# Optimization experiments

Hardware: AMD Instinct MI355X
Metric: run time of the kernel (lower is better)

Reference implementation:

```python
import jax, jax.numpy as jnp
import numpy as np
from jax import lax

ALPHA = 0.3          # opt['retrieval_strategy']['margin']
NB_SAMPLES = 10      # hardest negatives kept per anchor
W_IRR = 1.0
W_RII = 1.0
B = 4096
D = 1024
NB_CLASSES = 1048


def _pairwise_dist(x, y):
    # Euclidean pairwise distance matrix [B, B] (self.dist in the torch module)
    x2 = jnp.sum(x * x, axis=1, keepdims=True)          # [B,1]
    y2 = jnp.sum(y * y, axis=1, keepdims=True).T        # [1,B]
    d2 = x2 + y2 - 2.0 * (x @ y.T)
    return jnp.sqrt(jnp.maximum(d2, 0.0))


def setup_inputs() -> dict:
    key = jax.random.key(0)
    k1, k2, k3, k4 = jax.random.split(key, 4)
    input1 = jax.random.normal(k1, (B, D), dtype=jnp.float32)
    input2 = jax.random.normal(k2, (B, D), dtype=jnp.float32)
    # target==1 everywhere -> 'matches' mask selects the whole batch (identity gather)
    target = jnp.ones((B, 1), dtype=jnp.int32)
    # classes in [1, NB_CLASSES) -> all rows valid (class != 0)
    class1 = jax.random.randint(k3, (B, 1), 1, NB_CLASSES, dtype=jnp.int32)
    class2 = jax.random.randint(k4, (B, 1), 1, NB_CLASSES, dtype=jnp.int32)
    return {"input1": input1, "input2": input2, "target": target,
            "class1": class1, "class2": class2}


def _mine(cost):
    # calculate_cost with sampling='max_negative': sort rows descending, keep nb_samples.
    # top_k == descending sort truncated to k.
    top, _ = lax.top_k(cost, NB_SAMPLES)                # [B, NB_SAMPLES]
    return top


def reference(input1, input2, target, class1, class2):
    # matches = (target == 1) is all-true by construction -> instance_* = full inputs
    dist = _pairwise_dist(input1, input2)               # [B, B]
    diag = jnp.diagonal(dist)                           # [B]
    n = dist.shape[0]
    eye = jnp.eye(n, dtype=bool)

    # IRR: anchor image, positive its own recipe, negatives other recipes
    cost_irr = jnp.maximum(diag[:, None] - dist + ALPHA, 0.0)
    cost_irr = jnp.where(eye, 0.0, cost_irr)
    top_irr = _mine(cost_irr)
    bad_irr = jnp.mean((top_irr == 0.0).astype(jnp.float32))
    loss_irr = top_irr.mean() * W_IRR

    # RII: anchor recipe, positive its own image, negatives other images (cost.t())
    cost_rii = jnp.maximum(diag[None, :] - dist + ALPHA, 0.0)
    cost_rii = jnp.where(eye, 0.0, cost_rii)
    top_rii = _mine(cost_rii.T)
    bad_rii = jnp.mean((top_rii == 0.0).astype(jnp.float32))
    loss_rii = top_rii.mean() * W_RII

    return jnp.stack([loss_irr, loss_rii, bad_irr, bad_rii])
```

## Files before the change

### kernel.cpp

```cpp
#include <hip/hip_runtime.h>
#include <hip/hip_fp16.h>

#define ALPHA 0.3f
#define B_SZ 4096
#define D_SZ 1024
#define CT_STRIDE 137
#define BIGF 3.0e38f

typedef __attribute__((ext_vector_type(8))) _Float16 half8;
typedef __attribute__((ext_vector_type(4))) _Float16 half4;
typedef __attribute__((ext_vector_type(4))) float floatx4;

typedef __attribute__((address_space(1))) const void* gas_t;
typedef __attribute__((address_space(3))) void* las_t;

__device__ __forceinline__ float wave_reduce_add(float v) {
#pragma unroll
    for (int off = 32; off; off >>= 1) v += __shfl_xor(v, off);
    return v;
}

__device__ __forceinline__ void insert10(float (&best)[10], float x) {
#pragma unroll
    for (int p = 0; p < 10; ++p) {
        float lo = fminf(best[p], x);
        x = fmaxf(best[p], x);
        best[p] = lo;
    }
}

__global__ void __launch_bounds__(256) prep_kernel(
    const float* __restrict__ in1, const float* __restrict__ in2,
    _Float16* __restrict__ Xh, _Float16* __restrict__ Yh,
    float* __restrict__ x2, float* __restrict__ y2, float* __restrict__ mth) {
    int row = blockIdx.x;
    int t = threadIdx.x;
    const float4* a4 = (const float4*)(in1 + (size_t)row * D_SZ);
    const float4* b4 = (const float4*)(in2 + (size_t)row * D_SZ);
    float4 a = a4[t], b = b4[t];
    half4 ha = {(_Float16)a.x, (_Float16)a.y, (_Float16)a.z, (_Float16)a.w};
    half4 hb = {(_Float16)b.x, (_Float16)b.y, (_Float16)b.z, (_Float16)b.w};
    ((half4*)(Xh + (size_t)row * D_SZ))[t] = ha;
    ((half4*)(Yh + (size_t)row * D_SZ))[t] = hb;
    float sa = a.x * a.x + a.y * a.y + a.z * a.z + a.w * a.w;
    float sb = b.x * b.x + b.y * b.y + b.z * b.z + b.w * b.w;
    float d0 = a.x - b.x, d1 = a.y - b.y, d2v = a.z - b.z, d3 = a.w - b.w;
    float sd = d0 * d0 + d1 * d1 + d2v * d2v + d3 * d3;
    sa = wave_reduce_add(sa);
    sb = wave_reduce_add(sb);
    sd = wave_reduce_add(sd);
    __shared__ float red[3][4];
    int wave = t >> 6, lane = t & 63;
    if (lane == 0) { red[0][wave] = sa; red[1][wave] = sb; red[2][wave] = sd; }
    __syncthreads();
    if (t == 0) {
        x2[row] = red[0][0] + red[0][1] + red[0][2] + red[0][3];
        y2[row] = red[1][0] + red[1][1] + red[1][2] + red[1][3];
        mth[row] = sqrtf(red[2][0] + red[2][1] + red[2][2] + red[2][3]) + ALPHA;
    }
}

__global__ void __launch_bounds__(256, 4) gemm_topk_kernel(
    const _Float16* __restrict__ Xh, const _Float16* __restrict__ Yh,
    const float* __restrict__ x2, const float* __restrict__ y2,
    float* __restrict__ CandI, float* __restrict__ CandR) {
    __shared__ _Float16 smem[128 * CT_STRIDE];
    _Float16* As = smem;
    _Float16* Bs = smem + 4096;
    int tid = threadIdx.x;
    int wave = tid >> 6, lane = tid & 63;
    int waveR = wave >> 1, waveC = wave & 1;
    int bx = blockIdx.x, by = blockIdx.y;
    int q = lane >> 4, mrow = lane & 15;

    floatx4 acc[4][4] = {};

    int c0 = tid, c1 = 256 + tid;
    int r0 = c0 >> 2, q0 = (c0 & 3) ^ ((r0 >> 1) & 3);
    int r1 = c1 >> 2, q1 = (c1 & 3) ^ ((r1 >> 1) & 3);
    const _Float16* gA0 = Xh + (size_t)(by * 128 + r0) * D_SZ + q0 * 8;
    const _Float16* gB0 = Yh + (size_t)(bx * 128 + r0) * D_SZ + q0 * 8;
    const _Float16* gA1 = Xh + (size_t)(by * 128 + r1) * D_SZ + q1 * 8;
    const _Float16* gB1 = Yh + (size_t)(bx * 128 + r1) * D_SZ + q1 * 8;
    _Float16* la0 = &As[(wave * 64) * 8];
    _Float16* lb0 = &Bs[(wave * 64) * 8];
    _Float16* la1 = &As[(256 + wave * 64) * 8];
    _Float16* lb1 = &Bs[(256 + wave * 64) * 8];

    int aoff[4], boff[4];
#pragma unroll
    for (int mi = 0; mi < 4; ++mi) {
        int R = waveR * 64 + mi * 16 + mrow;
        aoff[mi] = R * 32 + (q ^ ((R >> 1) & 3)) * 8;
    }
#pragma unroll
    for (int ni = 0; ni < 4; ++ni) {
        int R = waveC * 64 + ni * 16 + mrow;
        boff[ni] = R * 32 + (q ^ ((R >> 1) & 3)) * 8;
    }

    for (int k0 = 0; k0 < D_SZ; k0 += 32) {
        __syncthreads();
        __builtin_amdgcn_global_load_lds((gas_t)(const void*)(gA0 + k0), (las_t)(void*)la0, 16, 0, 0);
        __builtin_amdgcn_global_load_lds((gas_t)(const void*)(gB0 + k0), (las_t)(void*)lb0, 16, 0, 0);
        __builtin_amdgcn_global_load_lds((gas_t)(const void*)(gA1 + k0), (las_t)(void*)la1, 16, 0, 0);
        __builtin_amdgcn_global_load_lds((gas_t)(const void*)(gB1 + k0), (las_t)(void*)lb1, 16, 0, 0);
        __syncthreads();
        half8 af[4], bf[4];
#pragma unroll
        for (int mi = 0; mi < 4; ++mi) af[mi] = *(const half8*)&As[aoff[mi]];
#pragma unroll
        for (int ni = 0; ni < 4; ++ni) bf[ni] = *(const half8*)&Bs[boff[ni]];
#pragma unroll
        for (int mi = 0; mi < 4; ++mi)
#pragma unroll
            for (int ni = 0; ni < 4; ++ni)
                acc[mi][ni] = __builtin_amdgcn_mfma_f32_16x16x32_f16(af[mi], bf[ni], acc[mi][ni], 0, 0, 0);
    }
    __syncthreads();

    _Float16* Ct = smem;
#pragma unroll
    for (int ni = 0; ni < 4; ++ni) {
        int lc = waveC * 64 + ni * 16 + mrow;
        float y2v = y2[bx * 128 + lc];
#pragma unroll
        for (int mi = 0; mi < 4; ++mi) {
            int lr0 = waveR * 64 + mi * 16 + q * 4;
            int gr0 = by * 128 + lr0;
            floatx4 v = acc[mi][ni];
            Ct[(lr0 + 0) * CT_STRIDE + lc] = (_Float16)(x2[gr0 + 0] + y2v - 2.0f * v[0]);
            Ct[(lr0 + 1) * CT_STRIDE + lc] = (_Float16)(x2[gr0 + 1] + y2v - 2.0f * v[1]);
            Ct[(lr0 + 2) * CT_STRIDE + lc] = (_Float16)(x2[gr0 + 2] + y2v - 2.0f * v[2]);
            Ct[(lr0 + 3) * CT_STRIDE + lc] = (_Float16)(x2[gr0 + 3] + y2v - 2.0f * v[3]);
        }
    }
    __syncthreads();

    {
        int rloc = wave * 32 + (lane & 31);
        int chalf = lane >> 5;
        int grow = by * 128 + rloc;
        int diagc = grow - bx * 128;
        float best[10];
#pragma unroll
        for (int i = 0; i < 10; ++i) best[i] = BIGF;
#pragma unroll 8
        for (int i = 0; i < 64; ++i) {
            int lc = chalf * 64 + i;
            float x = (float)Ct[rloc * CT_STRIDE + lc];
            if (lc == diagc) x = BIGF;
            insert10(best, x);
        }
        float* dst = CandI + ((size_t)grow * 32 + bx) * 20 + chalf * 10;
#pragma unroll
        for (int k = 0; k < 10; ++k) dst[k] = best[k];
    }

    {
        int cloc = wave * 32 + (lane & 31);
        int rhalf = lane >> 5;
        int gcol = bx * 128 + cloc;
        int diagr = gcol - by * 128;
        float best[10];
#pragma unroll
        for (int i = 0; i < 10; ++i) best[i] = BIGF;
#pragma unroll 8
        for (int i = 0; i < 64; ++i) {
            int lr = rhalf * 64 + i;
            float x = (float)Ct[lr * CT_STRIDE + cloc];
            if (lr == diagr) x = BIGF;
            insert10(best, x);
        }
        float* dst = CandR + ((size_t)gcol * 32 + by) * 20 + rhalf * 10;
#pragma unroll
        for (int k = 0; k < 10; ++k) dst[k] = best[k];
    }
}

__global__ void __launch_bounds__(256) merge_kernel(
    const float* __restrict__ CandI, const float* __restrict__ CandR,
    const float* __restrict__ mth,
    float* __restrict__ Srow, float* __restrict__ Zrow) {
    int wave = threadIdx.x >> 6, lane = threadIdx.x & 63;
    int r = blockIdx.x * 4 + wave;
    int row = r & (B_SZ - 1);
    const float* cp = ((r < B_SZ) ? CandI : CandR) + (size_t)row * 640;
    float best[10];
#pragma unroll
    for (int i = 0; i < 10; ++i) best[i] = BIGF;
#pragma unroll
    for (int j = 0; j < 10; ++j) insert10(best, cp[j * 64 + lane]);

    float mrow = mth[row];
    float s = 0.f, z = 0.f;
#pragma unroll
    for (int round = 0; round < 10; ++round) {
        float v0 = best[0];
        float g = v0;
#pragma unroll
        for (int off = 32; off; off >>= 1) g = fminf(g, __shfl_xor(g, off));
        unsigned long long ball = __ballot(v0 == g);
        int leader = __ffsll(ball) - 1;
        if (lane == leader) {
#pragma unroll
            for (int p = 0; p < 9; ++p) best[p] = best[p + 1];
            best[9] = BIGF;
        }
        float d = sqrtf(fmaxf(g, 0.f));
        float c = fmaxf(mrow - d, 0.f);
        s += c;
        z += (c == 0.f) ? 1.f : 0.f;
    }
    if (lane == 0) { Srow[r] = s; Zrow[r] = z; }
}

__global__ void __launch_bounds__(256) finalize_kernel(
    const float* __restrict__ Srow, const float* __restrict__ Zrow,
    float* __restrict__ out) {
    __shared__ float red[256][4];
    int t = threadIdx.x;
    float s0 = 0, s1 = 0, z0 = 0, z1 = 0;
#pragma unroll
    for (int k = 0; k < 8; ++k) {
        int i = k * 256 + t;
        float4 sv = ((const float4*)Srow)[i];
        float4 zv = ((const float4*)Zrow)[i];
        float ss = sv.x + sv.y + sv.z + sv.w;
        float zz = zv.x + zv.y + zv.z + zv.w;
        if (i < 1024) { s0 += ss; z0 += zz; } else { s1 += ss; z1 += zz; }
    }
    red[t][0] = s0; red[t][1] = s1; red[t][2] = z0; red[t][3] = z1;
    __syncthreads();
    for (int off = 128; off > 0; off >>= 1) {
        if (t < off) {
#pragma unroll
            for (int j = 0; j < 4; ++j) red[t][j] += red[t + off][j];
        }
        __syncthreads();
    }
    if (t == 0) {
        const float inv = 1.0f / (float)(B_SZ * 10);
        out[0] = red[0][0] * inv;
        out[1] = red[0][1] * inv;
        out[2] = red[0][2] * inv;
        out[3] = red[0][3] * inv;
    }
}

extern "C" void kernel_launch(void* const* d_in, const int* in_sizes, int n_in,
                              void* d_out, int out_size, void* d_ws, size_t ws_size,
                              hipStream_t stream) {
    const float* in1 = (const float*)d_in[0];
    const float* in2 = (const float*)d_in[1];
    float* out = (float*)d_out;

    char* ws = (char*)d_ws;
    const size_t MB = 1024 * 1024;
    _Float16* Xh = (_Float16*)(ws);
    _Float16* Yh = (_Float16*)(ws + 8 * MB);
    float* CandI = (float*)(ws + 16 * MB);
    float* CandR = (float*)(ws + 27 * MB);
    float* x2   = (float*)(ws + 38 * MB);
    float* y2   = x2 + B_SZ;
    float* mth  = y2 + B_SZ;
    float* Srow = mth + B_SZ;
    float* Zrow = Srow + 2 * B_SZ;
    const size_t needed = 38 * MB + (size_t)(3 * B_SZ + 4 * B_SZ) * sizeof(float);
    if (ws_size < needed) return;

    hipLaunchKernelGGL(prep_kernel, dim3(B_SZ), dim3(256), 0, stream,
                       in1, in2, Xh, Yh, x2, y2, mth);
    hipLaunchKernelGGL(gemm_topk_kernel, dim3(32, 32), dim3(256), 0, stream,
                       Xh, Yh, x2, y2, CandI, CandR);
    hipLaunchKernelGGL(merge_kernel, dim3(2048), dim3(256), 0, stream,
                       CandI, CandR, mth, Srow, Zrow);
    hipLaunchKernelGGL(finalize_kernel, dim3(1), dim3(256), 0, stream,
                       Srow, Zrow, out);
}
```

Measured before the change: 158.7 us.

## Double GEMM K-step, transpose epilogue tile, and store merged fp16 candidates

The GEMM main loop now loads 64-wide K slices per iteration with an 8-way XOR swizzle and runs two MFMA sub-steps per sync, halving the number of barriers. The epilogue writes the distance tile transposed using vectorized half4 stores. Each block merges the two half-row top-10 lists with a cross-lane shuffle and stores only 10 fp16 candidates per tile, which cuts candidate traffic and merge work by four times. The cost is more LDS per block (33KB), which may reduce occupancy, plus extra shuffle work in the epilogue.

```diff
diff --git a/kernel.cpp b/kernel.cpp
--- a/kernel.cpp
+++ b/kernel.cpp
@@ -4,7 +4,7 @@
 #define ALPHA 0.3f
 #define B_SZ 4096
 #define D_SZ 1024
-#define CT_STRIDE 137
+#define CT_STRIDE 132
 #define BIGF 3.0e38f
 
 typedef __attribute__((ext_vector_type(8))) _Float16 half8;
@@ -27,6 +27,10 @@
         x = fmaxf(best[p], x);
         best[p] = lo;
     }
+}
+
+__device__ __forceinline__ unsigned short h16(float x) {
+    return __builtin_bit_cast(unsigned short, (_Float16)x);
 }
 
 __global__ void __launch_bounds__(256) prep_kernel(
@@ -63,10 +67,10 @@
 __global__ void __launch_bounds__(256, 4) gemm_topk_kernel(
     const _Float16* __restrict__ Xh, const _Float16* __restrict__ Yh,
     const float* __restrict__ x2, const float* __restrict__ y2,
-    float* __restrict__ CandI, float* __restrict__ CandR) {
-    __shared__ _Float16 smem[128 * CT_STRIDE];
+    _Float16* __restrict__ CandI, _Float16* __restrict__ CandR) {
+    __shared__ _Float16 smem[16896];
     _Float16* As = smem;
-    _Float16* Bs = smem + 4096;
+    _Float16* Bs = smem + 8192;
     int tid = threadIdx.x;
     int wave = tid >> 6, lane = tid & 63;
     int waveR = wave >> 1, waveC = wave & 1;
@@ -75,47 +79,48 @@
 
     floatx4 acc[4][4] = {};
 
-    int c0 = tid, c1 = 256 + tid;
-    int r0 = c0 >> 2, q0 = (c0 & 3) ^ ((r0 >> 1) & 3);
-    int r1 = c1 >> 2, q1 = (c1 & 3) ^ ((r1 >> 1) & 3);
-    const _Float16* gA0 = Xh + (size_t)(by * 128 + r0) * D_SZ + q0 * 8;
-    const _Float16* gB0 = Yh + (size_t)(bx * 128 + r0) * D_SZ + q0 * 8;
-    const _Float16* gA1 = Xh + (size_t)(by * 128 + r1) * D_SZ + q1 * 8;
-    const _Float16* gB1 = Yh + (size_t)(bx * 128 + r1) * D_SZ + q1 * 8;
-    _Float16* la0 = &As[(wave * 64) * 8];
-    _Float16* lb0 = &Bs[(wave * 64) * 8];
-    _Float16* la1 = &As[(256 + wave * 64) * 8];
-    _Float16* lb1 = &Bs[(256 + wave * 64) * 8];
-
-    int aoff[4], boff[4];
+    const _Float16* gA[4];
+    _Float16* la[4];
+#pragma unroll
+    for (int i = 0; i < 4; ++i) {
+        int c = i * 256 + tid;
+        int r = c >> 3, sp = c & 7;
+        gA[i] = Xh + (size_t)(by * 128 + r) * D_SZ + (sp ^ (r & 7)) * 8;
+        la[i] = &As[(i * 256 + wave * 64) * 8];
+    }
+    const ptrdiff_t bdelta = (Yh + (size_t)bx * 128 * D_SZ) - (Xh + (size_t)by * 128 * D_SZ);
+
+    int aoff[2][4];
 #pragma unroll
     for (int mi = 0; mi < 4; ++mi) {
         int R = waveR * 64 + mi * 16 + mrow;
-        aoff[mi] = R * 32 + (q ^ ((R >> 1) & 3)) * 8;
-    }
-#pragma unroll
-    for (int ni = 0; ni < 4; ++ni) {
-        int R = waveC * 64 + ni * 16 + mrow;
-        boff[ni] = R * 32 + (q ^ ((R >> 1) & 3)) * 8;
-    }
-
-    for (int k0 = 0; k0 < D_SZ; k0 += 32) {
+        int Rx = R & 7;
+        aoff[0][mi] = R * 64 + (q ^ Rx) * 8;
+        aoff[1][mi] = R * 64 + ((q + 4) ^ Rx) * 8;
+    }
+    const int bdel = (waveC - waveR) * 64 * 64;
+
+    for (int k0 = 0; k0 < D_SZ; k0 += 64) {
         __syncthreads();
-        __builtin_amdgcn_global_load_lds((gas_t)(const void*)(gA0 + k0), (las_t)(void*)la0, 16, 0, 0);
-        __builtin_amdgcn_global_load_lds((gas_t)(const void*)(gB0 + k0), (las_t)(void*)lb0, 16, 0, 0);
-        __builtin_amdgcn_global_load_lds((gas_t)(const void*)(gA1 + k0), (las_t)(void*)la1, 16, 0, 0);
-        __builtin_amdgcn_global_load_lds((gas_t)(const void*)(gB1 + k0), (las_t)(void*)lb1, 16, 0, 0);
+#pragma unroll
+        for (int i = 0; i < 4; ++i) {
+            __builtin_amdgcn_global_load_lds((gas_t)(const void*)(gA[i] + k0), (las_t)(void*)la[i], 16, 0, 0);
+            __builtin_amdgcn_global_load_lds((gas_t)(const void*)(gA[i] + bdelta + k0), (las_t)(void*)(la[i] + 8192), 16, 0, 0);
+        }
         __syncthreads();
-        half8 af[4], bf[4];
-#pragma unroll
-        for (int mi = 0; mi < 4; ++mi) af[mi] = *(const half8*)&As[aoff[mi]];
-#pragma unroll
-        for (int ni = 0; ni < 4; ++ni) bf[ni] = *(const half8*)&Bs[boff[ni]];
-#pragma unroll
-        for (int mi = 0; mi < 4; ++mi)
-#pragma unroll
-            for (int ni = 0; ni < 4; ++ni)
-                acc[mi][ni] = __builtin_amdgcn_mfma_f32_16x16x32_f16(af[mi], bf[ni], acc[mi][ni], 0, 0, 0);
+#pragma unroll
+        for (int ks = 0; ks < 2; ++ks) {
+            half8 af[4], bf[4];
+#pragma unroll
+            for (int mi = 0; mi < 4; ++mi) af[mi] = *(const half8*)&As[aoff[ks][mi]];
+#pragma unroll
+            for (int ni = 0; ni < 4; ++ni) bf[ni] = *(const half8*)&Bs[aoff[ks][ni] + bdel];
+#pragma unroll
+            for (int mi = 0; mi < 4; ++mi)
+#pragma unroll
+                for (int ni = 0; ni < 4; ++ni)
+                    acc[mi][ni] = __builtin_amdgcn_mfma_f32_16x16x32_f16(af[mi], bf[ni], acc[mi][ni], 0, 0, 0);
+        }
     }
     __syncthreads();
 
@@ -129,10 +134,11 @@
             int lr0 = waveR * 64 + mi * 16 + q * 4;
             int gr0 = by * 128 + lr0;
             floatx4 v = acc[mi][ni];
-            Ct[(lr0 + 0) * CT_STRIDE + lc] = (_Float16)(x2[gr0 + 0] + y2v - 2.0f * v[0]);
-            Ct[(lr0 + 1) * CT_STRIDE + lc] = (_Float16)(x2[gr0 + 1] + y2v - 2.0f * v[1]);
-            Ct[(lr0 + 2) * CT_STRIDE + lc] = (_Float16)(x2[gr0 + 2] + y2v - 2.0f * v[2]);
-            Ct[(lr0 + 3) * CT_STRIDE + lc] = (_Float16)(x2[gr0 + 3] + y2v - 2.0f * v[3]);
+            half4 hv = {(_Float16)(x2[gr0 + 0] + y2v - 2.0f * v[0]),
+                        (_Float16)(x2[gr0 + 1] + y2v - 2.0f * v[1]),
+                        (_Float16)(x2[gr0 + 2] + y2v - 2.0f * v[2]),
+                        (_Float16)(x2[gr0 + 3] + y2v - 2.0f * v[3])};
+            *(half4*)&Ct[lc * CT_STRIDE + lr0] = hv;
         }
     }
     __syncthreads();
@@ -148,13 +154,21 @@
 #pragma unroll 8
         for (int i = 0; i < 64; ++i) {
             int lc = chalf * 64 + i;
-            float x = (float)Ct[rloc * CT_STRIDE + lc];
+            float x = (float)Ct[lc * CT_STRIDE + rloc];
             if (lc == diagc) x = BIGF;
             insert10(best, x);
         }
-        float* dst = CandI + ((size_t)grow * 32 + bx) * 20 + chalf * 10;
-#pragma unroll
-        for (int k = 0; k < 10; ++k) dst[k] = best[k];
+        float tmp[10];
+#pragma unroll
+        for (int k = 0; k < 10; ++k) tmp[k] = __shfl_xor(best[k], 32);
+#pragma unroll
+        for (int k = 0; k < 10; ++k) insert10(best, tmp[k]);
+        if (lane < 32) {
+            unsigned int* dst = (unsigned int*)CandI + ((size_t)grow * 32 + bx) * 5;
+#pragma unroll
+            for (int k = 0; k < 5; ++k)
+                dst[k] = (unsigned int)h16(best[2 * k]) | ((unsigned int)h16(best[2 * k + 1]) << 16);
+        }
     }
 
     {
@@ -168,29 +182,37 @@
 #pragma unroll 8
         for (int i = 0; i < 64; ++i) {
             int lr = rhalf * 64 + i;
-            float x = (float)Ct[lr * CT_STRIDE + cloc];
+            float x = (float)Ct[cloc * CT_STRIDE + lr];
             if (lr == diagr) x = BIGF;
             insert10(best, x);
         }
-        float* dst = CandR + ((size_t)gcol * 32 + by) * 20 + rhalf * 10;
-#pragma unroll
-        for (int k = 0; k < 10; ++k) dst[k] = best[k];
+        float tmp[10];
+#pragma unroll
+        for (int k = 0; k < 10; ++k) tmp[k] = __shfl_xor(best[k], 32);
+#pragma unroll
+        for (int k = 0; k < 10; ++k) insert10(best, tmp[k]);
+        if (lane < 32) {
+            unsigned int* dst = (unsigned int*)CandR + ((size_t)gcol * 32 + by) * 5;
+#pragma unroll
+            for (int k = 0; k < 5; ++k)
+                dst[k] = (unsigned int)h16(best[2 * k]) | ((unsigned int)h16(best[2 * k + 1]) << 16);
+        }
     }
 }
 
 __global__ void __launch_bounds__(256) merge_kernel(
-    const float* __restrict__ CandI, const float* __restrict__ CandR,
+    const _Float16* __restrict__ CandI, const _Float16* __restrict__ CandR,
     const float* __restrict__ mth,
     float* __restrict__ Srow, float* __restrict__ Zrow) {
     int wave = threadIdx.x >> 6, lane = threadIdx.x & 63;
     int r = blockIdx.x * 4 + wave;
     int row = r & (B_SZ - 1);
-    const float* cp = ((r < B_SZ) ? CandI : CandR) + (size_t)row * 640;
+    const _Float16* cp = ((r < B_SZ) ? CandI : CandR) + (size_t)row * 320;
     float best[10];
 #pragma unroll
     for (int i = 0; i < 10; ++i) best[i] = BIGF;
 #pragma unroll
-    for (int j = 0; j < 10; ++j) insert10(best, cp[j * 64 + lane]);
+    for (int j = 0; j < 5; ++j) insert10(best, (float)cp[j * 64 + lane]);
 
     float mrow = mth[row];
     float s = 0.f, z = 0.f;
@@ -259,14 +281,14 @@
     const size_t MB = 1024 * 1024;
     _Float16* Xh = (_Float16*)(ws);
     _Float16* Yh = (_Float16*)(ws + 8 * MB);
-    float* CandI = (float*)(ws + 16 * MB);
-    float* CandR = (float*)(ws + 27 * MB);
-    float* x2   = (float*)(ws + 38 * MB);
+    _Float16* CandI = (_Float16*)(ws + 16 * MB);
+    _Float16* CandR = (_Float16*)(ws + 19 * MB);
+    float* x2   = (float*)(ws + 22 * MB);
     float* y2   = x2 + B_SZ;
     float* mth  = y2 + B_SZ;
     float* Srow = mth + B_SZ;
     float* Zrow = Srow + 2 * B_SZ;
-    const size_t needed = 38 * MB + (size_t)(3 * B_SZ + 4 * B_SZ) * sizeof(float);
+    const size_t needed = 22 * MB + (size_t)(3 * B_SZ + 4 * B_SZ) * sizeof(float);
     if (ws_size < needed) return;
 
     hipLaunchKernelGGL(prep_kernel, dim3(B_SZ), dim3(256), 0, stream,
```

Measured after the change: 167.4 us. 1.05x slower.

## Use packed half2 top-10 selection with fp16 candidates and transposed tile

Applied to the files above, without the earlier changes.

Stores the distance tile transposed and runs the per-row and per-column top-10 insertion networks on packed half2 values, so each lane handles two rows or column halves per min/max instruction. The diagonal is masked once with a sentinel write instead of a compare on every element. Candidates are written as 10 fp16 values per tile instead of 20 floats, which shrinks candidate traffic and merge-kernel reads. The risk is fp16 precision in the candidate ordering and more complex shuffle and merge logic.

```diff
diff --git a/kernel.cpp b/kernel.cpp
--- a/kernel.cpp
+++ b/kernel.cpp
@@ -4,11 +4,13 @@
 #define ALPHA 0.3f
 #define B_SZ 4096
 #define D_SZ 1024
-#define CT_STRIDE 137
+#define CT_STRIDE 132
 #define BIGF 3.0e38f
+#define SENT_F 60000.0f
 
 typedef __attribute__((ext_vector_type(8))) _Float16 half8;
 typedef __attribute__((ext_vector_type(4))) _Float16 half4;
+typedef __attribute__((ext_vector_type(2))) _Float16 half2v;
 typedef __attribute__((ext_vector_type(4))) float floatx4;
 
 typedef __attribute__((address_space(1))) const void* gas_t;
@@ -27,6 +29,19 @@
         x = fmaxf(best[p], x);
         best[p] = lo;
     }
+}
+
+__device__ __forceinline__ void insert10p(half2v (&b)[10], half2v x) {
+#pragma unroll
+    for (int p = 0; p < 10; ++p) {
+        half2v lo = __builtin_elementwise_min(b[p], x);
+        x = __builtin_elementwise_max(b[p], x);
+        b[p] = lo;
+    }
+}
+
+__device__ __forceinline__ unsigned short h16(float x) {
+    return __builtin_bit_cast(unsigned short, (_Float16)x);
 }
 
 __global__ void __launch_bounds__(256) prep_kernel(
@@ -63,8 +78,8 @@
 __global__ void __launch_bounds__(256, 4) gemm_topk_kernel(
     const _Float16* __restrict__ Xh, const _Float16* __restrict__ Yh,
     const float* __restrict__ x2, const float* __restrict__ y2,
-    float* __restrict__ CandI, float* __restrict__ CandR) {
-    __shared__ _Float16 smem[128 * CT_STRIDE];
+    _Float16* __restrict__ CandI, _Float16* __restrict__ CandR) {
+    __shared__ _Float16 smem[16896];
     _Float16* As = smem;
     _Float16* Bs = smem + 4096;
     int tid = threadIdx.x;
@@ -129,68 +144,86 @@
             int lr0 = waveR * 64 + mi * 16 + q * 4;
             int gr0 = by * 128 + lr0;
             floatx4 v = acc[mi][ni];
-            Ct[(lr0 + 0) * CT_STRIDE + lc] = (_Float16)(x2[gr0 + 0] + y2v - 2.0f * v[0]);
-            Ct[(lr0 + 1) * CT_STRIDE + lc] = (_Float16)(x2[gr0 + 1] + y2v - 2.0f * v[1]);
-            Ct[(lr0 + 2) * CT_STRIDE + lc] = (_Float16)(x2[gr0 + 2] + y2v - 2.0f * v[2]);
-            Ct[(lr0 + 3) * CT_STRIDE + lc] = (_Float16)(x2[gr0 + 3] + y2v - 2.0f * v[3]);
-        }
-    }
-    __syncthreads();
-
-    {
-        int rloc = wave * 32 + (lane & 31);
+            half4 hv = {(_Float16)(x2[gr0 + 0] + y2v - 2.0f * v[0]),
+                        (_Float16)(x2[gr0 + 1] + y2v - 2.0f * v[1]),
+                        (_Float16)(x2[gr0 + 2] + y2v - 2.0f * v[2]),
+                        (_Float16)(x2[gr0 + 3] + y2v - 2.0f * v[3])};
+            *(half4*)&Ct[lc * CT_STRIDE + lr0] = hv;
+        }
+    }
+    __syncthreads();
+    if (bx == by && tid < 128) Ct[tid * CT_STRIDE + tid] = (_Float16)SENT_F;
+    __syncthreads();
+
+    const half2v sent2 = {(_Float16)SENT_F, (_Float16)SENT_F};
+
+    if (wave < 2) {
+        int p = wave * 32 + (lane & 31);
         int chalf = lane >> 5;
-        int grow = by * 128 + rloc;
-        int diagc = grow - bx * 128;
-        float best[10];
-#pragma unroll
-        for (int i = 0; i < 10; ++i) best[i] = BIGF;
+        half2v b[10];
+#pragma unroll
+        for (int i = 0; i < 10; ++i) b[i] = sent2;
 #pragma unroll 8
         for (int i = 0; i < 64; ++i) {
-            int lc = chalf * 64 + i;
-            float x = (float)Ct[rloc * CT_STRIDE + lc];
-            if (lc == diagc) x = BIGF;
-            insert10(best, x);
-        }
-        float* dst = CandI + ((size_t)grow * 32 + bx) * 20 + chalf * 10;
-#pragma unroll
-        for (int k = 0; k < 10; ++k) dst[k] = best[k];
-    }
-
-    {
-        int cloc = wave * 32 + (lane & 31);
-        int rhalf = lane >> 5;
-        int gcol = bx * 128 + cloc;
-        int diagr = gcol - by * 128;
-        float best[10];
-#pragma unroll
-        for (int i = 0; i < 10; ++i) best[i] = BIGF;
+            int c = chalf * 64 + i;
+            half2v v = *(const half2v*)&Ct[c * CT_STRIDE + 2 * p];
+            insert10p(b, v);
+        }
+        half2v t[10];
+#pragma unroll
+        for (int k = 0; k < 10; ++k)
+            t[k] = __builtin_bit_cast(half2v, __shfl_xor(__builtin_bit_cast(int, b[k]), 32));
+#pragma unroll
+        for (int k = 0; k < 10; ++k) insert10p(b, t[k]);
+        if (lane < 32) {
+            int grow = by * 128 + 2 * p;
+            unsigned int* d0 = (unsigned int*)CandI + ((size_t)grow * 32 + bx) * 5;
+            unsigned int* d1 = d0 + 32 * 5;
+#pragma unroll
+            for (int k = 0; k < 5; ++k) {
+                unsigned int u0 = __builtin_bit_cast(unsigned int, b[2 * k]);
+                unsigned int u1 = __builtin_bit_cast(unsigned int, b[2 * k + 1]);
+                d0[k] = (u0 & 0xFFFFu) | (u1 << 16);
+                d1[k] = (u0 >> 16) | (u1 & 0xFFFF0000u);
+            }
+        }
+    } else {
+        int c = (wave - 2) * 64 + lane;
+        half2v b[10];
+#pragma unroll
+        for (int i = 0; i < 10; ++i) b[i] = sent2;
+        const half2v* colp = (const half2v*)&Ct[c * CT_STRIDE];
 #pragma unroll 8
-        for (int i = 0; i < 64; ++i) {
-            int lr = rhalf * 64 + i;
-            float x = (float)Ct[lr * CT_STRIDE + cloc];
-            if (lr == diagr) x = BIGF;
-            insert10(best, x);
-        }
-        float* dst = CandR + ((size_t)gcol * 32 + by) * 20 + rhalf * 10;
-#pragma unroll
-        for (int k = 0; k < 10; ++k) dst[k] = best[k];
+        for (int i = 0; i < 64; ++i) insert10p(b, colp[i]);
+        float bf[10];
+#pragma unroll
+        for (int i = 0; i < 10; ++i) bf[i] = BIGF;
+#pragma unroll
+        for (int k = 0; k < 10; ++k) {
+            insert10(bf, (float)b[k][0]);
+            insert10(bf, (float)b[k][1]);
+        }
+        int gcol = bx * 128 + c;
+        unsigned int* d = (unsigned int*)CandR + ((size_t)gcol * 32 + by) * 5;
+#pragma unroll
+        for (int k = 0; k < 5; ++k)
+            d[k] = (unsigned int)h16(bf[2 * k]) | ((unsigned int)h16(bf[2 * k + 1]) << 16);
     }
 }
 
 __global__ void __launch_bounds__(256) merge_kernel(
-    const float* __restrict__ CandI, const float* __restrict__ CandR,
+    const _Float16* __restrict__ CandI, const _Float16* __restrict__ CandR,
     const float* __restrict__ mth,
     float* __restrict__ Srow, float* __restrict__ Zrow) {
     int wave = threadIdx.x >> 6, lane = threadIdx.x & 63;
     int r = blockIdx.x * 4 + wave;
     int row = r & (B_SZ - 1);
-    const float* cp = ((r < B_SZ) ? CandI : CandR) + (size_t)row * 640;
+    const _Float16* cp = ((r < B_SZ) ? CandI : CandR) + (size_t)row * 320;
     float best[10];
 #pragma unroll
     for (int i = 0; i < 10; ++i) best[i] = BIGF;
 #pragma unroll
-    for (int j = 0; j < 10; ++j) insert10(best, cp[j * 64 + lane]);
+    for (int j = 0; j < 5; ++j) insert10(best, (float)cp[j * 64 + lane]);
 
     float mrow = mth[row];
     float s = 0.f, z = 0.f;
@@ -259,14 +292,14 @@
     const size_t MB = 1024 * 1024;
     _Float16* Xh = (_Float16*)(ws);
     _Float16* Yh = (_Float16*)(ws + 8 * MB);
-    float* CandI = (float*)(ws + 16 * MB);
-    float* CandR = (float*)(ws + 27 * MB);
-    float* x2   = (float*)(ws + 38 * MB);
+    _Float16* CandI = (_Float16*)(ws + 16 * MB);
+    _Float16* CandR = (_Float16*)(ws + 19 * MB);
+    float* x2   = (float*)(ws + 22 * MB);
     float* y2   = x2 + B_SZ;
     float* mth  = y2 + B_SZ;
     float* Srow = mth + B_SZ;
     float* Zrow = Srow + 2 * B_SZ;
-    const size_t needed = 38 * MB + (size_t)(3 * B_SZ + 4 * B_SZ) * sizeof(float);
+    const size_t needed = 22 * MB + (size_t)(3 * B_SZ + 4 * B_SZ) * sizeof(float);
     if (ws_size < needed) return;
 
     hipLaunchKernelGGL(prep_kernel, dim3(B_SZ), dim3(256), 0, stream,
```

Measured after the change: 147.0 us. -7.4%, faster.
